# Performance work log

Hardware: AMD Instinct MI355X
Metric: run time of the kernel (lower is better)

## Reference

```python
import jax, jax.numpy as jnp
import numpy as np

B, S, E, H = 2, 2048, 1024, 16
HD = E // H
SCALE = 1.0 / np.sqrt(HD)
PR_QKV = 0.05   # precision_ratio for q/k/v (critical_attention=False)
PR_OUT = 0.10
ROUTE_THR = 0.05  # gradient_threshold (critical_attention=False)
LN_EPS = 1e-5


def rpb_linear(x, W, b, precision_ratio):
    """ResidualPrecisionBoostLinear: ternary-quantized weight (threshold 0.7*mean|W|,
    per-tensor scale) plus top-`precision_ratio` fraction of residual kept full precision."""
    absW = jnp.abs(W)
    thr = 0.7 * jnp.mean(absW)
    tmask = (absW > thr).astype(W.dtype)
    scale = jnp.sum(absW * tmask) / jnp.maximum(jnp.sum(tmask), 1.0)
    Wq = scale * jnp.sign(W) * tmask
    res = W - Wq
    k = int(precision_ratio * W.size)
    kth = jax.lax.top_k(jnp.abs(res).ravel(), k)[0][-1]
    W_eff = Wq + res * (jnp.abs(res) >= kth).astype(W.dtype)
    return x @ W_eff.T + b


def selective_route(x, threshold):
    # forward: zero out small-magnitude activations (straight-through in training)
    return x * (jnp.abs(x) >= threshold).astype(x.dtype)


def layer_norm(x, g, b):
    mu = jnp.mean(x, axis=-1, keepdims=True)
    var = jnp.mean(jnp.square(x - mu), axis=-1, keepdims=True)
    return (x - mu) * jax.lax.rsqrt(var + LN_EPS) * g + b


def setup_inputs() -> dict:
    key = jax.random.key(0)
    ks = jax.random.split(key, 12)
    f = lambda k, shp, s=1.0: jax.random.normal(k, shp, dtype=jnp.float32) * s
    return {
        "query": f(ks[0], (B, S, E)),
        "key": f(ks[1], (B, S, E)),
        "value": f(ks[2], (B, S, E)),
        "Wq": f(ks[3], (E, E), 0.02), "bq": jnp.zeros((E,), jnp.float32),
        "Wk": f(ks[4], (E, E), 0.02), "bk": jnp.zeros((E,), jnp.float32),
        "Wv": f(ks[5], (E, E), 0.02), "bv": jnp.zeros((E,), jnp.float32),
        "Wo": f(ks[6], (E, E), 0.02), "bo": jnp.zeros((E,), jnp.float32),
        "ln_g": jnp.ones((E,), jnp.float32),
        "ln_b": jnp.zeros((E,), jnp.float32),
    }


def reference(query, key, value, Wq, bq, Wk, bk, Wv, bv, Wo, bo, ln_g, ln_b):
    qn = layer_norm(query, ln_g, ln_b)
    q = selective_route(rpb_linear(qn, Wq, bq, PR_QKV), ROUTE_THR)
    k = selective_route(rpb_linear(key, Wk, bk, PR_QKV), ROUTE_THR)
    v = selective_route(rpb_linear(value, Wv, bv, PR_QKV), ROUTE_THR)
    # [B,S,E] -> [B,H,S,HD]
    q = q.reshape(B, S, H, HD).transpose(0, 2, 1, 3)
    k = k.reshape(B, S, H, HD).transpose(0, 2, 1, 3)
    v = v.reshape(B, S, H, HD).transpose(0, 2, 1, 3)
    scores = jnp.einsum("bhqd,bhkd->bhqk", q, k) * SCALE
    attn = jax.nn.softmax(scores, axis=-1)   # dropout is identity in eval
    ctx = jnp.einsum("bhqk,bhkd->bhqd", attn, v)
    ctx = ctx.transpose(0, 2, 1, 3).reshape(B, S, E)
    return rpb_linear(ctx, Wo, bo, PR_OUT)
```

## Files before the change

### kernel.cpp

```cpp
#include <hip/hip_runtime.h>
#include <stdio.h>
#include <stdint.h>

#define BB 2
#define SS 2048
#define ED 1024
#define HH 16
#define HDD 64
#define MROWS 4096
#define NW_ELEM 1048576u

typedef unsigned short ushortT;
typedef __attribute__((ext_vector_type(8))) short bf16x8;
typedef __attribute__((ext_vector_type(4))) float f32x4;
typedef __attribute__((ext_vector_type(16))) float f32x16;

#define U_WHI 0u
#define U_WLO 4194304u
#define U_XQ  8388608u
#define U_XK  12582912u
#define U_XV  16777216u
#define U_QH  20971520u
#define U_KH  25165824u
#define U_VH  29360128u
#define LP_OFF  33554432u
#define P0_OFF  67108864u
#define P1_OFF  83886080u
#define SMALL_OFF  100663296u
#define HIST_OFF   SMALL_OFF
#define ABS_OFF    (SMALL_OFF + 16384u)
#define MSK_OFF    (ABS_OFF + 32u)
#define CNT_OFF    (MSK_OFF + 32u)
#define SMALL_BYTES 16464u
#define WS_NEEDED  (SMALL_OFF + SMALL_BYTES)

#define SC44 17592186044416.0f
#define INV44 (1.0 / 17592186044416.0)
#define QSCALE 0.18033688011112042f

__device__ __forceinline__ const float* wsel(int w, const float* W0, const float* W1,
                                             const float* W2, const float* W3) {
  return w == 0 ? W0 : w == 1 ? W1 : w == 2 ? W2 : W3;
}

__device__ __forceinline__ ushortT f2bf(float x) {
  unsigned u = __float_as_uint(x);
  unsigned r = (u + 0x7FFFu + ((u >> 16) & 1u)) >> 16;
  return (ushortT)r;
}
__device__ __forceinline__ float bf2f(ushortT b) {
  return __uint_as_float(((unsigned)b) << 16);
}
__device__ __forceinline__ void bsplit(float x, ushortT& h, ushortT& l) {
  ushortT hb = f2bf(x);
  float hf = bf2f(hb);
  h = hb;
  l = f2bf(x - hf);
}
__device__ __forceinline__ unsigned pkbf(float a, float b) {
  unsigned r;
  asm("v_cvt_pk_bf16_f32 %0, %1, %2" : "=v"(r) : "v"(a), "v"(b));
  return r;
}
__device__ __forceinline__ void plswap(unsigned& a, unsigned& b) {
  asm("v_permlane32_swap_b32 %0, %1" : "+v"(a), "+v"(b));
}

__device__ __forceinline__ void gld_lds16(const ushortT* g, ushortT* s) {
  __builtin_amdgcn_global_load_lds((__attribute__((address_space(1))) void*)g,
                                   (__attribute__((address_space(3))) void*)s, 16, 0, 0);
}

template <int N> __device__ __forceinline__ void waitv() {
  if constexpr (N == 0) asm volatile("s_waitcnt vmcnt(0)" ::: "memory");
  else if constexpr (N == 4) asm volatile("s_waitcnt vmcnt(4)" ::: "memory");
  else if constexpr (N == 6) asm volatile("s_waitcnt vmcnt(6)" ::: "memory");
}
__device__ __forceinline__ void pipe_barrier() {
  __builtin_amdgcn_s_barrier();
  __builtin_amdgcn_sched_barrier(0);
}

__device__ __forceinline__ float get_thr(const unsigned long long* sAbs, int w) {
  return 0.7f * (float)((double)sAbs[w] * INV44 / 1048576.0);
}
__device__ __forceinline__ float get_scale(const unsigned long long* sMsk,
                                           const unsigned* cnt, int w) {
  double s = (double)sMsk[w] * INV44;
  return (float)s / fmaxf((float)cnt[w], 1.0f);
}

__device__ __forceinline__ void scan_sel(const unsigned* hist, unsigned& k, unsigned& prefix,
                                         unsigned* sh, int t) {
  sh[t] = hist[t];
  __syncthreads();
  for (int off = 1; off < 256; off <<= 1) {
    unsigned add = (t + off < 256) ? sh[t + off] : 0u;
    __syncthreads();
    sh[t] += add;
    __syncthreads();
  }
  int sel = __syncthreads_count((int)(sh[t] >= k)) - 1;
  unsigned suf = sh[sel];
  k -= (suf - hist[sel]);
  prefix = (prefix << 8) | (unsigned)sel;
  __syncthreads();
}

__global__ __launch_bounds__(256) void k_wstats(const float* W0, const float* W1,
                                                const float* W2, const float* W3,
                                                unsigned long long* sAbs) {
  const int w = blockIdx.y, t = threadIdx.x;
  const float* W = wsel(w, W0, W1, W2, W3) + blockIdx.x * 4096;
  unsigned long long s = 0;
#pragma unroll
  for (int r = 0; r < 4; r++) {
    float4 v = *(const float4*)(W + (t + 256 * r) * 4);
    s += (unsigned long long)(fabsf(v.x) * SC44);
    s += (unsigned long long)(fabsf(v.y) * SC44);
    s += (unsigned long long)(fabsf(v.z) * SC44);
    s += (unsigned long long)(fabsf(v.w) * SC44);
  }
  __shared__ unsigned long long sd[256];
  sd[t] = s;
  __syncthreads();
  for (int off = 128; off > 0; off >>= 1) {
    if (t < off) sd[t] += sd[t + off];
    __syncthreads();
  }
  if (!t) atomicAdd(&sAbs[w], sd[0]);
}

__global__ __launch_bounds__(256) void k_masked(const float* W0, const float* W1,
                                                const float* W2, const float* W3,
                                                const unsigned long long* sAbs,
                                                unsigned long long* sMsk, unsigned* sCnt) {
  const int w = blockIdx.y, t = threadIdx.x;
  const float thr = get_thr(sAbs, w);
  const float* W = wsel(w, W0, W1, W2, W3) + blockIdx.x * 4096;
  unsigned long long s = 0;
  unsigned c = 0;
#pragma unroll
  for (int r = 0; r < 4; r++) {
    float4 v = *(const float4*)(W + (t + 256 * r) * 4);
    float xs[4] = {v.x, v.y, v.z, v.w};
#pragma unroll
    for (int q = 0; q < 4; q++) {
      float a = fabsf(xs[q]);
      if (a > thr) { s += (unsigned long long)(a * SC44); c++; }
    }
  }
  __shared__ unsigned long long sd[256];
  __shared__ unsigned sc[256];
  sd[t] = s; sc[t] = c;
  __syncthreads();
  for (int off = 128; off > 0; off >>= 1) {
    if (t < off) { sd[t] += sd[t + off]; sc[t] += sc[t + off]; }
    __syncthreads();
  }
  if (!t) { atomicAdd(&sMsk[w], sd[0]); atomicAdd(&sCnt[w], sc[0]); }
}

__global__ __launch_bounds__(256) void k_hist(const float* W0, const float* W1,
                                              const float* W2, const float* W3,
                                              const unsigned long long* sAbs,
                                              const unsigned long long* sMsk,
                                              const unsigned* sCnt,
                                              unsigned* histG, int pass) {
  const int w = blockIdx.y, t = threadIdx.x;
  __shared__ unsigned sh[256];
  __shared__ unsigned h[256];
  const float thr = get_thr(sAbs, w);
  const float scale = get_scale(sMsk, sCnt, w);
  unsigned k = (w == 3) ? 104857u : 52428u, prefix = 0u;
  for (int pp = 0; pp < pass; pp++)
    scan_sel(histG + (pp * 4 + w) * 256, k, prefix, sh, t);

  h[t] = 0;
  __syncthreads();
  const float* W = wsel(w, W0, W1, W2, W3) + blockIdx.x * 4096;
  const int shift1 = 32 - 8 * pass;
  const int shift2 = 24 - 8 * pass;
#pragma unroll
  for (int r = 0; r < 4; r++) {
    float4 v = *(const float4*)(W + (t + 256 * r) * 4);
    float xs[4] = {v.x, v.y, v.z, v.w};
#pragma unroll
    for (int q = 0; q < 4; q++) {
      float x = xs[q];
      float a = fabsf(x);
      float wq = (a > thr) ? copysignf(scale, x) : 0.0f;
      unsigned bits = __float_as_uint(fabsf(x - wq));
      if (pass == 0) {
        atomicAdd(&h[bits >> 24], 1u);
      } else {
        if ((bits >> shift1) == prefix)
          atomicAdd(&h[(bits >> shift2) & 255u], 1u);
      }
    }
  }
  __syncthreads();
  if (h[t]) atomicAdd(&histG[(pass * 4 + w) * 256 + t], h[t]);
}

__global__ __launch_bounds__(256) void k_weff(const float* W0, const float* W1,
                                              const float* W2, const float* W3,
                                              const unsigned long long* sAbs,
                                              const unsigned long long* sMsk,
                                              const unsigned* sCnt,
                                              const unsigned* histG,
                                              ushortT* Whi, ushortT* Wlo) {
  const int w = blockIdx.y, t = threadIdx.x;
  __shared__ unsigned sh[256];
  const float thr = get_thr(sAbs, w);
  const float scale = get_scale(sMsk, sCnt, w);
  unsigned k = (w == 3) ? 104857u : 52428u, kth = 0u;
  for (int pp = 0; pp < 4; pp++)
    scan_sel(histG + (pp * 4 + w) * 256, k, kth, sh, t);

  const unsigned idx = (blockIdx.x * 256 + t) * 4;
  const float* W = wsel(w, W0, W1, W2, W3);
  float4 v = *(const float4*)(W + idx);
  float xs[4] = {v.x, v.y, v.z, v.w};
  ushort4 h4, l4;
#pragma unroll
  for (int c = 0; c < 4; c++) {
    float x = xs[c];
    float a = fabsf(x);
    float wq = (a > thr) ? copysignf(scale, x) : 0.0f;
    float res = x - wq;
    unsigned bits = __float_as_uint(fabsf(res));
    float we = wq + ((bits >= kth) ? res : 0.0f);
    ushortT hh, ll;
    bsplit(we, hh, ll);
    ((ushortT*)&h4)[c] = hh;
    ((ushortT*)&l4)[c] = ll;
  }
  *(ushort4*)&Whi[(size_t)w * NW_ELEM + idx] = h4;
  *(ushort4*)&Wlo[(size_t)w * NW_ELEM + idx] = l4;
}

__global__ __launch_bounds__(256) void k_pre(const float* __restrict__ query,
                                             const float* __restrict__ key,
                                             const float* __restrict__ value,
                                             const float* __restrict__ g,
                                             const float* __restrict__ b,
                                             ushortT* __restrict__ Xq,
                                             ushortT* __restrict__ Xk,
                                             ushortT* __restrict__ Xv) {
  const int t = threadIdx.x;
  if (blockIdx.y == 0) {
    const int row = blockIdx.x;
    __shared__ float red[8];
    float4 v = *(const float4*)&query[(size_t)row * ED + t * 4];
    float s = v.x + v.y + v.z + v.w;
#pragma unroll
    for (int m = 32; m; m >>= 1) s += __shfl_xor(s, m, 64);
    if ((t & 63) == 0) red[t >> 6] = s;
    __syncthreads();
    float mu = (red[0] + red[1] + red[2] + red[3]) * (1.0f / 1024.0f);
    float dx = v.x - mu, dy = v.y - mu, dz = v.z - mu, dw = v.w - mu;
    float s2 = dx * dx + dy * dy + dz * dz + dw * dw;
#pragma unroll
    for (int m = 32; m; m >>= 1) s2 += __shfl_xor(s2, m, 64);
    if ((t & 63) == 0) red[4 + (t >> 6)] = s2;
    __syncthreads();
    float var = (red[4] + red[5] + red[6] + red[7]) * (1.0f / 1024.0f);
    float inv = rsqrtf(var + 1e-5f);
    float4 gg = *(const float4*)&g[t * 4];
    float4 bb = *(const float4*)&b[t * 4];
    float ys[4] = {dx * inv * gg.x + bb.x, dy * inv * gg.y + bb.y,
                   dz * inv * gg.z + bb.z, dw * inv * gg.w + bb.w};
    ushort4 h4;
#pragma unroll
    for (int c = 0; c < 4; c++) ((ushortT*)&h4)[c] = f2bf(ys[c]);
    *(ushort4*)&Xq[(size_t)row * ED + t * 4] = h4;
  } else {
    const float* src = (blockIdx.y == 1) ? key : value;
    ushortT* dst = (blockIdx.y == 1) ? Xk : Xv;
    const int i = (blockIdx.x * 256 + t) * 4;
    float4 v = *(const float4*)&src[i];
    ushort4 h4;
    h4.x = f2bf(v.x); h4.y = f2bf(v.y); h4.z = f2bf(v.z); h4.w = f2bf(v.w);
    *(ushort4*)&dst[i] = h4;
  }
}

__device__ __forceinline__ f32x4 mfma16(bf16x8 a, bf16x8 b, f32x4 c) {
  return __builtin_amdgcn_mfma_f32_16x16x32_bf16(a, b, c, 0, 0, 0);
}

template <int MODE, bool ALO, bool WLO, int BK, int MINW>
__global__ __launch_bounds__(256, MINW) void k_gemmP(
    const ushortT* __restrict__ A0, const ushortT* __restrict__ A0l,
    const ushortT* __restrict__ A1,
    const ushortT* __restrict__ Wh, const ushortT* __restrict__ Wl,
    const float* __restrict__ bias0, const float* __restrict__ bias1,
    ushortT* __restrict__ Cb0, ushortT* __restrict__ Cb1,
    float* __restrict__ Cf) {
  constexpr int ABUF = (BK == 64) ? 8192 : 4096;
  constexpr int BBUF = (BK == 64) ? 4096 : 2048;
  constexpr int L = ((BK == 64) ? 4 : 2) * (1 + (ALO ? 1 : 0)) +
                    ((BK == 64) ? 2 : 1) * (1 + (WLO ? 1 : 0));
  constexpr int NT = 1024 / BK;
  __shared__ __align__(16) ushortT sAh[3 * ABUF];
  __shared__ __align__(16) ushortT sAl[ALO ? 3 * ABUF : 8];
  __shared__ __align__(16) ushortT sBh[3 * BBUF];
  __shared__ __align__(16) ushortT sBl[WLO ? 3 * BBUF : 8];

  const int t = threadIdx.x;
  const int w = t >> 6, l = t & 63;
  const int wr = w >> 1, wc = w & 1;

  const int which = (MODE == 0) ? (blockIdx.x >> 9) : 0;
  const int wid = blockIdx.x & 511;
  int id2 = (wid & 7) * 64 + (wid >> 3);
  const int m0 = (id2 >> 4) * 128, n0 = (id2 & 15) * 64;

  const ushortT* A = (MODE == 0 && which) ? A1 : A0;
  const ushortT* Wha = Wh + (MODE == 0 ? (unsigned)which * NW_ELEM : 0u);
  const float* bias = (MODE == 0 && which) ? bias1 : bias0;

  const int sr = l >> 3, swz = (l & 7) ^ sr;
  const int srow = l >> 2, sgr = (l & 3) ^ ((l >> 3) & 3);

  auto stage = [&](int kt, int buf) {
    if constexpr (BK == 64) {
#pragma unroll
      for (int s2 = 0; s2 < 4; s2++) {
        int seg = w * 4 + s2;
        size_t ga = (size_t)(m0 + seg * 8 + sr) * ED + kt * 64 + swz * 8;
        gld_lds16(A + ga, sAh + buf * ABUF + seg * 512);
        if constexpr (ALO) gld_lds16(A0l + ga, sAl + buf * ABUF + seg * 512);
      }
#pragma unroll
      for (int s2 = 0; s2 < 2; s2++) {
        int seg = w * 2 + s2;
        size_t gb = (size_t)(n0 + seg * 8 + sr) * ED + kt * 64 + swz * 8;
        gld_lds16(Wha + gb, sBh + buf * BBUF + seg * 512);
        if constexpr (WLO) gld_lds16(Wl + gb, sBl + buf * BBUF + seg * 512);
      }
    } else {
#pragma unroll
      for (int s2 = 0; s2 < 2; s2++) {
        int seg = w * 2 + s2;
        size_t ga = (size_t)(m0 + seg * 16 + srow) * ED + kt * 32 + sgr * 8;
        gld_lds16(A + ga, sAh + buf * ABUF + seg * 512);
        if constexpr (ALO) gld_lds16(A0l + ga, sAl + buf * ABUF + seg * 512);
      }
      {
        size_t gb = (size_t)(n0 + w * 16 + srow) * ED + kt * 32 + sgr * 8;
        gld_lds16(Wha + gb, sBh + buf * BBUF + w * 512);
        if constexpr (WLO) gld_lds16(Wl + gb, sBl + buf * BBUF + w * 512);
      }
    }
  };

  f32x4 acc[4][2];
#pragma unroll
  for (int i = 0; i < 4; i++)
#pragma unroll
    for (int j = 0; j < 2; j++) acc[i][j] = (f32x4){0.0f, 0.0f, 0.0f, 0.0f};

  auto compute = [&](int buf) {
    if constexpr (BK == 64) {
#pragma unroll
      for (int ks = 0; ks < 2; ks++) {
        bf16x8 ah[4], al[4], bh2[2], bl2[2];
        const int G = ks * 4 + (l >> 4);
#pragma unroll
        for (int i = 0; i < 4; i++) {
          int r = wr * 64 + i * 16 + (l & 15);
          int off = buf * ABUF + r * 64 + ((G ^ (l & 7)) << 3);
          ah[i] = *(const bf16x8*)&sAh[off];
          if constexpr (ALO) al[i] = *(const bf16x8*)&sAl[off];
        }
#pragma unroll
        for (int j = 0; j < 2; j++) {
          int r = wc * 32 + j * 16 + (l & 15);
          int off = buf * BBUF + r * 64 + ((G ^ (l & 7)) << 3);
          bh2[j] = *(const bf16x8*)&sBh[off];
          if constexpr (WLO) bl2[j] = *(const bf16x8*)&sBl[off];
        }
#pragma unroll
        for (int i = 0; i < 4; i++)
#pragma unroll
          for (int j = 0; j < 2; j++) {
            acc[i][j] = mfma16(ah[i], bh2[j], acc[i][j]);
            if constexpr (WLO) acc[i][j] = mfma16(ah[i], bl2[j], acc[i][j]);
            if constexpr (ALO) acc[i][j] = mfma16(al[i], bh2[j], acc[i][j]);
          }
      }
    } else {
      bf16x8 ah[4], al[4], bh2[2], bl2[2];
      const int G = l >> 4;
#pragma unroll
      for (int i = 0; i < 4; i++) {
        int r = wr * 64 + i * 16 + (l & 15);
        int off = buf * ABUF + r * 32 + ((G ^ ((r >> 1) & 3)) << 3);
        ah[i] = *(const bf16x8*)&sAh[off];
        if constexpr (ALO) al[i] = *(const bf16x8*)&sAl[off];
      }
#pragma unroll
      for (int j = 0; j < 2; j++) {
        int r = wc * 32 + j * 16 + (l & 15);
        int off = buf * BBUF + r * 32 + ((G ^ ((r >> 1) & 3)) << 3);
        bh2[j] = *(const bf16x8*)&sBh[off];
        if constexpr (WLO) bl2[j] = *(const bf16x8*)&sBl[off];
      }
#pragma unroll
      for (int i = 0; i < 4; i++)
#pragma unroll
        for (int j = 0; j < 2; j++) {
          acc[i][j] = mfma16(ah[i], bh2[j], acc[i][j]);
          if constexpr (WLO) acc[i][j] = mfma16(ah[i], bl2[j], acc[i][j]);
          if constexpr (ALO) acc[i][j] = mfma16(al[i], bh2[j], acc[i][j]);
        }
    }
  };

  stage(0, 0);
  stage(1, 1);
  for (int kt = 0; kt < NT; ++kt) {
    if (kt < NT - 1) waitv<L>(); else waitv<0>();
    pipe_barrier();
    if (kt + 2 < NT) stage(kt + 2, (kt + 2) % 3);
    __builtin_amdgcn_s_setprio(1);
    compute(kt % 3);
    __builtin_amdgcn_s_setprio(0);
  }

  const int coln = l & 15, row4 = (l >> 4) * 4;
  float bn[2];
#pragma unroll
  for (int j = 0; j < 2; j++) bn[j] = bias[n0 + wc * 32 + j * 16 + coln];
  const int b_ = m0 >> 11, h_ = n0 >> 6;

  if constexpr (MODE == 1) {
#pragma unroll
    for (int i = 0; i < 4; i++)
#pragma unroll
      for (int j = 0; j < 2; j++) {
        int n = n0 + wc * 32 + j * 16 + coln;
#pragma unroll
        for (int r = 0; r < 4; r++) {
          int m = m0 + wr * 64 + i * 16 + row4 + r;
          Cf[(size_t)m * ED + n] = acc[i][j][r] + bn[j];
        }
      }
  } else if constexpr (MODE == 0) {
    const float osc = (which == 0) ? QSCALE : 1.0f;
    ushortT* C = which ? Cb1 : Cb0;
#pragma unroll
    for (int i = 0; i < 4; i++)
#pragma unroll
      for (int j = 0; j < 2; j++) {
        int hd = wc * 32 + j * 16 + coln;
#pragma unroll
        for (int r = 0; r < 4; r++) {
          int m = m0 + wr * 64 + i * 16 + row4 + r;
          int s_ = m & 2047;
          float y = acc[i][j][r] + bn[j];
          y = (fabsf(y) >= 0.05f) ? y : 0.0f;
          y *= osc;
          C[((size_t)(b_ * HH + h_) * SS + s_) * HDD + hd] = f2bf(y);
        }
      }
  } else {
#pragma unroll
    for (int i = 0; i < 4; i++)
#pragma unroll
      for (int j = 0; j < 2; j++) {
        int hd = wc * 32 + j * 16 + coln;
        int s0_ = (m0 + wr * 64 + i * 16 + row4) & 2047;
        ushort4 h4;
#pragma unroll
        for (int r = 0; r < 4; r++) {
          float y = acc[i][j][r] + bn[j];
          y = (fabsf(y) >= 0.05f) ? y : 0.0f;
          ((ushortT*)&h4)[r] = f2bf(y);
        }
        *(ushort4*)&Cb0[((size_t)(b_ * HH + h_) * HDD + hd) * SS + s0_] = h4;
      }
  }
}

__device__ __forceinline__ f32x16 mfma32(bf16x8 a, bf16x8 b, f32x16 c) {
  return __builtin_amdgcn_mfma_f32_32x32x16_bf16(a, b, c, 0, 0, 0);
}

__device__ __forceinline__ void exppack(const f32x16& A, float& lsum,
                                        bf16x8& paA, bf16x8& paB) {
  float p[16];
#pragma unroll
  for (int r = 0; r < 16; r++) {
    p[r] = exp2f(A[r]);
    lsum += p[r];
  }
  unsigned c0 = pkbf(p[0], p[1]), c1 = pkbf(p[2], p[3]);
  unsigned c2 = pkbf(p[4], p[5]), c3 = pkbf(p[6], p[7]);
  unsigned c4 = pkbf(p[8], p[9]), c5 = pkbf(p[10], p[11]);
  unsigned c6 = pkbf(p[12], p[13]), c7 = pkbf(p[14], p[15]);
  plswap(c0, c2); plswap(c1, c3); plswap(c4, c6); plswap(c5, c7);
  uint4 ta = make_uint4(c0, c1, c2, c3);
  uint4 tb = make_uint4(c4, c5, c6, c7);
  paA = __builtin_bit_cast(bf16x8, ta);
  paB = __builtin_bit_cast(bf16x8, tb);
}

__global__ __launch_bounds__(256, 3) void k_attn(
    const ushortT* __restrict__ Qh, const ushortT* __restrict__ Kh,
    const ushortT* __restrict__ Vh,
    float* __restrict__ Pp, float* __restrict__ Lp) {
  __shared__ __align__(16) ushortT sK[3 * 4096];
  __shared__ __align__(16) ushortT sV[3 * 4096];

  const int t = threadIdx.x;
  const int w = t >> 6, l = t & 63;
  const int l32 = l & 31, g = l >> 5;

  int id = blockIdx.x;
  int id2 = (id & 7) * 128 + (id >> 3);
  const int bh = id2 >> 5;
  const int qt = (id2 >> 1) & 15;
  const int half = id2 & 1;

  const size_t kqbase = (size_t)bh * (SS * HDD);
  const size_t vbase = (size_t)bh * (HDD * SS);
  const int q0 = qt * 128 + w * 32;
  const int sbase = half * 1024;

  bf16x8 qh[4];
  const size_t qrow = kqbase + (size_t)(q0 + l32) * HDD;
#pragma unroll
  for (int ks = 0; ks < 4; ks++) qh[ks] = *(const bf16x8*)&Qh[qrow + ks * 16 + g * 8];

  f32x16 octx0, octx1;
#pragma unroll
  for (int i = 0; i < 16; i++) { octx0[i] = 0.0f; octx1[i] = 0.0f; }
  float lsum = 0.0f;

  const int srow = l >> 3;
  const int sgr = (l & 7) ^ srow;

  auto stageA = [&](int kt, int buf) {
    const int s0 = sbase + kt * 64;
#pragma unroll
    for (int s2 = 0; s2 < 2; s2++) {
      int seg = w * 2 + s2;
      int row = seg * 8 + srow;
      gld_lds16(Kh + kqbase + (size_t)(s0 + row) * HDD + sgr * 8, sK + buf * 4096 + seg * 512);
      gld_lds16(Vh + vbase + (size_t)row * SS + s0 + sgr * 8, sV + buf * 4096 + seg * 512);
    }
  };

  stageA(0, 0);
  stageA(1, 1);

  for (int kt = 0; kt < 16; ++kt) {
    if (kt < 15) waitv<4>(); else waitv<0>();
    pipe_barrier();
    if (kt + 2 < 16) stageA(kt + 2, (kt + 2) % 3);
    const ushortT* cK = sK + (kt % 3) * 4096;
    const ushortT* cV = sV + (kt % 3) * 4096;

    f32x16 acc0, acc1;
#pragma unroll
    for (int i = 0; i < 16; i++) { acc0[i] = 0.0f; acc1[i] = 0.0f; }
    __builtin_amdgcn_s_setprio(1);
#pragma unroll
    for (int ks = 0; ks < 4; ks++) {
      int sw = ((ks * 2 + g) ^ (l32 & 7)) << 3;
      bf16x8 kh0 = *(const bf16x8*)&cK[l32 * 64 + sw];
      bf16x8 kh1 = *(const bf16x8*)&cK[(32 + l32) * 64 + sw];
      acc0 = mfma32(kh0, qh[ks], acc0);
      acc1 = mfma32(kh1, qh[ks], acc1);
    }
    __builtin_amdgcn_s_setprio(0);

    bf16x8 pa0, pa1, pa2, pa3;
    exppack(acc0, lsum, pa0, pa1);
    exppack(acc1, lsum, pa2, pa3);

    __builtin_amdgcn_s_setprio(1);
#pragma unroll
    for (int js = 0; js < 4; js++) {
      bf16x8 pj = js == 0 ? pa0 : js == 1 ? pa1 : js == 2 ? pa2 : pa3;
      int vsw = ((js * 2 + g) ^ (l32 & 7)) << 3;
      bf16x8 vh0 = *(const bf16x8*)&cV[l32 * 64 + vsw];
      bf16x8 vh1 = *(const bf16x8*)&cV[(32 + l32) * 64 + vsw];
      octx0 = mfma32(pj, vh0, octx0);
      octx1 = mfma32(pj, vh1, octx1);
    }
    __builtin_amdgcn_s_setprio(0);
  }

  float ls = lsum + __shfl_xor(lsum, 32, 64);
  if (g == 0) Lp[half * 65536 + bh * 2048 + q0 + l32] = ls;

  float* P = Pp + (size_t)half * 4194304u;
#pragma unroll
  for (int r = 0; r < 16; r++) {
    int q = (r & 3) + 8 * (r >> 2) + 4 * g;
    size_t pb = ((size_t)bh * 2048 + q0 + q) * 64;
    P[pb + l32] = octx0[r];
    P[pb + 32 + l32] = octx1[r];
  }
}

__global__ __launch_bounds__(256) void k_reduce(const float* __restrict__ Pp,
                                                const float* __restrict__ Lp,
                                                ushortT* __restrict__ ctxH,
                                                ushortT* __restrict__ ctxL) {
  const unsigned i4 = (blockIdx.x * 256 + threadIdx.x) * 4;
  const int d = i4 & 63;
  const int sq = (i4 >> 6) & 2047;
  const int bh = i4 >> 17;
  float ls = Lp[bh * 2048 + sq] + Lp[65536 + bh * 2048 + sq];
  float inv = 1.0f / ls;
  float4 a = *(const float4*)&Pp[i4];
  float4 b = *(const float4*)&Pp[4194304u + i4];
  float os[4] = {(a.x + b.x) * inv, (a.y + b.y) * inv,
                 (a.z + b.z) * inv, (a.w + b.w) * inv};
  ushort4 h4, l4;
#pragma unroll
  for (int c = 0; c < 4; c++) {
    ushortT hh, ll;
    bsplit(os[c], hh, ll);
    ((ushortT*)&h4)[c] = hh;
    ((ushortT*)&l4)[c] = ll;
  }
  size_t ci = ((size_t)((bh >> 4) * 2048 + sq)) * 1024 + (bh & 15) * 64 + d;
  *(ushort4*)&ctxH[ci] = h4;
  *(ushort4*)&ctxL[ci] = l4;
}

extern "C" void kernel_launch(void* const* d_in, const int* in_sizes, int n_in,
                              void* d_out, int out_size, void* d_ws, size_t ws_size,
                              hipStream_t stream) {
  const float* query = (const float*)d_in[0];
  const float* key   = (const float*)d_in[1];
  const float* value = (const float*)d_in[2];
  const float* Wq = (const float*)d_in[3];
  const float* bq = (const float*)d_in[4];
  const float* Wk = (const float*)d_in[5];
  const float* bk = (const float*)d_in[6];
  const float* Wv = (const float*)d_in[7];
  const float* bv = (const float*)d_in[8];
  const float* Wo = (const float*)d_in[9];
  const float* bo = (const float*)d_in[10];
  const float* lng = (const float*)d_in[11];
  const float* lnb = (const float*)d_in[12];
  float* out = (float*)d_out;

  if (ws_size < (size_t)WS_NEEDED) {
    fprintf(stderr, "kernel_launch: ws too small (%zu < %u)\n", ws_size, WS_NEEDED);
    return;
  }

  ushortT* wsu = (ushortT*)d_ws;
  ushortT* Whi = wsu + U_WHI;
  ushortT* Wlo = wsu + U_WLO;
  ushortT* Xq  = wsu + U_XQ;
  ushortT* Xk  = wsu + U_XK;
  ushortT* Xv  = wsu + U_XV;
  ushortT* Qhp = wsu + U_QH;
  ushortT* Khp = wsu + U_KH;
  ushortT* Vhp = wsu + U_VH;
  ushortT* Chp = wsu + U_XQ;
  ushortT* Clp = wsu + U_XK;

  char* wsb = (char*)d_ws;
  float* Pp = (float*)(wsb + P0_OFF);
  float* Lp = (float*)(wsb + LP_OFF);
  unsigned* histG = (unsigned*)(wsb + HIST_OFF);
  unsigned long long* sAbs = (unsigned long long*)(wsb + ABS_OFF);
  unsigned long long* sMsk = (unsigned long long*)(wsb + MSK_OFF);
  unsigned* sCnt = (unsigned*)(wsb + CNT_OFF);

  hipMemsetAsync(histG, 0, SMALL_BYTES, stream);

  k_pre<<<dim3(MROWS, 3), 256, 0, stream>>>(query, key, value, lng, lnb, Xq, Xk, Xv);

  dim3 gW(256, 4);
  k_wstats<<<gW, 256, 0, stream>>>(Wq, Wk, Wv, Wo, sAbs);
  k_masked<<<gW, 256, 0, stream>>>(Wq, Wk, Wv, Wo, sAbs, sMsk, sCnt);
  for (int pass = 0; pass < 4; ++pass)
    k_hist<<<gW, 256, 0, stream>>>(Wq, Wk, Wv, Wo, sAbs, sMsk, sCnt, histG, pass);
  k_weff<<<dim3(1024, 4), 256, 0, stream>>>(Wq, Wk, Wv, Wo, sAbs, sMsk, sCnt, histG,
                                            Whi, Wlo);

  k_gemmP<0, false, false, 64, 2><<<1024, 256, 0, stream>>>(
      Xq, nullptr, Xk, Whi, nullptr, bq, bk, Qhp, Khp, nullptr);
  k_gemmP<2, false, true, 32, 3><<<512, 256, 0, stream>>>(
      Xv, nullptr, nullptr, Whi + 2 * NW_ELEM, Wlo + 2 * NW_ELEM, bv, nullptr,
      Vhp, nullptr, nullptr);

  k_attn<<<1024, 256, 0, stream>>>(Qhp, Khp, Vhp, Pp, Lp);
  k_reduce<<<4096, 256, 0, stream>>>(Pp, Lp, Chp, Clp);

  k_gemmP<1, true, true, 32, 2><<<512, 256, 0, stream>>>(
      Chp, Clp, nullptr, Whi + 3 * NW_ELEM, Wlo + 3 * NW_ELEM, bo, nullptr,
      nullptr, nullptr, out);
}
```

Before: 258.3 us.

## Switch attention K/V staging to double-buffer, raise occupancy, use raw exp2

The attention kernel's K/V shared-memory staging drops from a triple-buffered pipeline with explicit vmcnt waits to a simpler double buffer synchronized by __syncthreads. Shared memory per block shrinks, and the launch bound asks for 4 blocks per CU instead of 3. It also swaps exp2f for the hardware exp2 intrinsic, splits the row-sum into four independent accumulators to shorten the dependency chain, and removes the s_setprio hints. The trade-off is less prefetch distance and a full barrier every iteration in exchange for more resident waves and cheaper exponentials.

```diff
diff --git a/kernel.cpp b/kernel.cpp
--- a/kernel.cpp
+++ b/kernel.cpp
@@ -65,6 +65,15 @@
 __device__ __forceinline__ void plswap(unsigned& a, unsigned& b) {
   asm("v_permlane32_swap_b32 %0, %1" : "+v"(a), "+v"(b));
 }
+__device__ __forceinline__ float fexp2(float x) {
+#if __has_builtin(__builtin_amdgcn_exp2f)
+  return __builtin_amdgcn_exp2f(x);
+#else
+  float r;
+  asm("v_exp_f32 %0, %1\n\ts_nop 1" : "=v"(r) : "v"(x));
+  return r;
+#endif
+}
 
 __device__ __forceinline__ void gld_lds16(const ushortT* g, ushortT* s) {
   __builtin_amdgcn_global_load_lds((__attribute__((address_space(1))) void*)g,
@@ -489,13 +498,13 @@
   return __builtin_amdgcn_mfma_f32_32x32x16_bf16(a, b, c, 0, 0, 0);
 }
 
-__device__ __forceinline__ void exppack(const f32x16& A, float& lsum,
+__device__ __forceinline__ void exppack(const f32x16& A, float* ls4,
                                         bf16x8& paA, bf16x8& paB) {
   float p[16];
 #pragma unroll
   for (int r = 0; r < 16; r++) {
-    p[r] = exp2f(A[r]);
-    lsum += p[r];
+    p[r] = fexp2(A[r]);
+    ls4[r & 3] += p[r];
   }
   unsigned c0 = pkbf(p[0], p[1]), c1 = pkbf(p[2], p[3]);
   unsigned c2 = pkbf(p[4], p[5]), c3 = pkbf(p[6], p[7]);
@@ -508,12 +517,12 @@
   paB = __builtin_bit_cast(bf16x8, tb);
 }
 
-__global__ __launch_bounds__(256, 3) void k_attn(
+__global__ __launch_bounds__(256, 4) void k_attn(
     const ushortT* __restrict__ Qh, const ushortT* __restrict__ Kh,
     const ushortT* __restrict__ Vh,
     float* __restrict__ Pp, float* __restrict__ Lp) {
-  __shared__ __align__(16) ushortT sK[3 * 4096];
-  __shared__ __align__(16) ushortT sV[3 * 4096];
+  __shared__ __align__(16) ushortT sK[2 * 4096];
+  __shared__ __align__(16) ushortT sV[2 * 4096];
 
   const int t = threadIdx.x;
   const int w = t >> 6, l = t & 63;
@@ -538,7 +547,7 @@
   f32x16 octx0, octx1;
 #pragma unroll
   for (int i = 0; i < 16; i++) { octx0[i] = 0.0f; octx1[i] = 0.0f; }
-  float lsum = 0.0f;
+  float ls4[4] = {0.0f, 0.0f, 0.0f, 0.0f};
 
   const int srow = l >> 3;
   const int sgr = (l & 7) ^ srow;
@@ -555,19 +564,16 @@
   };
 
   stageA(0, 0);
-  stageA(1, 1);
+  __syncthreads();
 
   for (int kt = 0; kt < 16; ++kt) {
-    if (kt < 15) waitv<4>(); else waitv<0>();
-    pipe_barrier();
-    if (kt + 2 < 16) stageA(kt + 2, (kt + 2) % 3);
-    const ushortT* cK = sK + (kt % 3) * 4096;
-    const ushortT* cV = sV + (kt % 3) * 4096;
+    if (kt < 15) stageA(kt + 1, (kt + 1) & 1);
+    const ushortT* cK = sK + (kt & 1) * 4096;
+    const ushortT* cV = sV + (kt & 1) * 4096;
 
     f32x16 acc0, acc1;
 #pragma unroll
     for (int i = 0; i < 16; i++) { acc0[i] = 0.0f; acc1[i] = 0.0f; }
-    __builtin_amdgcn_s_setprio(1);
 #pragma unroll
     for (int ks = 0; ks < 4; ks++) {
       int sw = ((ks * 2 + g) ^ (l32 & 7)) << 3;
@@ -576,13 +582,11 @@
       acc0 = mfma32(kh0, qh[ks], acc0);
       acc1 = mfma32(kh1, qh[ks], acc1);
     }
-    __builtin_amdgcn_s_setprio(0);
 
     bf16x8 pa0, pa1, pa2, pa3;
-    exppack(acc0, lsum, pa0, pa1);
-    exppack(acc1, lsum, pa2, pa3);
-
-    __builtin_amdgcn_s_setprio(1);
+    exppack(acc0, ls4, pa0, pa1);
+    exppack(acc1, ls4, pa2, pa3);
+
 #pragma unroll
     for (int js = 0; js < 4; js++) {
       bf16x8 pj = js == 0 ? pa0 : js == 1 ? pa1 : js == 2 ? pa2 : pa3;
@@ -592,9 +596,10 @@
       octx0 = mfma32(pj, vh0, octx0);
       octx1 = mfma32(pj, vh1, octx1);
     }
-    __builtin_amdgcn_s_setprio(0);
-  }
-
+    __syncthreads();
+  }
+
+  float lsum = (ls4[0] + ls4[1]) + (ls4[2] + ls4[3]);
   float ls = lsum + __shfl_xor(lsum, 32, 64);
   if (g == 0) Lp[half * 65536 + bh * 2048 + q0 + l32] = ls;
 
```

After: 241.7 us. 1.07x faster.
